# Kernel tuning notes

Hardware: AMD Instinct MI355X
Metric: run time of the kernel (lower is better)

The kernel has to match this reference:

```python
import jax, jax.numpy as jnp
import numpy as np

N_NODES = 100000
N_EDGES = 1600000
N_FEAT = 500
N_CLASSES = 40


def gcn_conv(x, W, b, src, dst, n):
    """PyG GCNConv: add self-loops, symmetric deg normalization, linear + bias."""
    h = x @ W                                   # [n, out]
    loop = jnp.arange(n, dtype=src.dtype)
    s = jnp.concatenate([src, loop])            # sources incl. self-loops
    d = jnp.concatenate([dst, loop])            # destinations incl. self-loops
    deg = jax.ops.segment_sum(jnp.ones_like(d, dtype=x.dtype), d, num_segments=n)
    dinv = jax.lax.rsqrt(deg)                   # deg >= 1 because of self-loops
    norm = dinv[s] * dinv[d]                    # [E+n]
    out = jax.ops.segment_sum(h[s] * norm[:, None], d, num_segments=n)
    return out + b


def glorot(key, fan_in, fan_out):
    lim = np.sqrt(6.0 / (fan_in + fan_out)).astype(np.float32)
    return jax.random.uniform(key, (fan_in, fan_out), jnp.float32, -lim, lim)


def setup_inputs() -> dict:
    key = jax.random.key(0)
    ks = jax.random.split(key, 6)
    x = jax.random.normal(ks[0], (N_NODES, N_FEAT), dtype=jnp.float32)
    edge_index = jax.random.randint(ks[1], (2, N_EDGES), 0, N_NODES, dtype=jnp.int64)
    return {
        "x": x,
        "edge_index": edge_index,
        "W1": glorot(ks[2], N_FEAT, 128), "b1": jnp.zeros((128,), jnp.float32),
        "W2": glorot(ks[3], 128, 64),     "b2": jnp.zeros((64,), jnp.float32),
        "W4": glorot(ks[4], 64, N_CLASSES), "b4": jnp.zeros((N_CLASSES,), jnp.float32),
    }


def reference(x, edge_index, W1, b1, W2, b2, W4, b4):
    src, dst = edge_index[0], edge_index[1]
    n = x.shape[0]
    h = jax.nn.relu(gcn_conv(x, W1, b1, src, dst, n))
    h = jax.nn.relu(gcn_conv(h, W2, b2, src, dst, n))
    h = gcn_conv(h, W4, b4, src, dst, n)
    return jax.nn.log_softmax(h, axis=1)
```

## Files before the change

### kernel.cpp

```cpp
#include <hip/hip_runtime.h>
#include <hip/hip_bf16.h>
#include <cmath>

#define NNODES 100000
#define NEDGES 1600000
#define SCAN_B 1024

typedef __attribute__((ext_vector_type(8))) short bf16x8;
typedef __attribute__((ext_vector_type(4))) float f32x4;

__device__ __forceinline__ unsigned short f2bf(float f) {
    unsigned u = __builtin_bit_cast(unsigned, f);
    unsigned r = (u + 0x7fffu + ((u >> 16) & 1u)) >> 16;
    return (unsigned short)r;
}
__device__ __forceinline__ float bflo(unsigned v) {
    return __builtin_bit_cast(float, v << 16);
}
__device__ __forceinline__ float bfhi(unsigned v) {
    return __builtin_bit_cast(float, v & 0xffff0000u);
}


__global__ void zero_deg(int* __restrict__ deg, int n) {
    int i = blockIdx.x * 256 + threadIdx.x;
    if (i < n) deg[i] = 0;
}

__global__ void count_deg(const int* __restrict__ dst, int* __restrict__ deg, int E) {
    int e = blockIdx.x * 256 + threadIdx.x;
    if (e < E) atomicAdd(&deg[dst[e]], 1);
}

__global__ void calc_dinv(const int* __restrict__ deg, float* __restrict__ dinv, int n) {
    int i = blockIdx.x * 256 + threadIdx.x;
    if (i < n) dinv[i] = rsqrtf(1.0f + (float)deg[i]);
}

__global__ __launch_bounds__(SCAN_B) void scan_block(const int* __restrict__ deg,
                                                     int* __restrict__ pos,
                                                     int* __restrict__ bsums, int n) {
    __shared__ int s[SCAN_B];
    int tid = threadIdx.x;
    int gid = blockIdx.x * SCAN_B + tid;
    int v = (gid < n) ? deg[gid] : 0;
    s[tid] = v;
    __syncthreads();
    for (int off = 1; off < SCAN_B; off <<= 1) {
        int t = (tid >= off) ? s[tid - off] : 0;
        __syncthreads();
        s[tid] += t;
        __syncthreads();
    }
    if (gid < n) pos[gid] = s[tid] - v;
    if (tid == SCAN_B - 1) bsums[blockIdx.x] = s[tid];
}

__global__ __launch_bounds__(128) void scan_sums(int* __restrict__ bsums, int nb) {
    __shared__ int s[128];
    int tid = threadIdx.x;
    int v = (tid < nb) ? bsums[tid] : 0;
    s[tid] = v;
    __syncthreads();
    for (int off = 1; off < 128; off <<= 1) {
        int t = (tid >= off) ? s[tid - off] : 0;
        __syncthreads();
        s[tid] += t;
        __syncthreads();
    }
    if (tid < nb) bsums[tid] = s[tid] - v;
}

__global__ __launch_bounds__(SCAN_B) void add_off(int* __restrict__ pos,
                                                  const int* __restrict__ bsums, int n) {
    int gid = blockIdx.x * SCAN_B + threadIdx.x;
    if (gid < n) pos[gid] += bsums[blockIdx.x];
}

__global__ void csr_fill(const int* __restrict__ src, const int* __restrict__ dst,
                         int* __restrict__ pos, int* __restrict__ csr_src, int E) {
    int e = blockIdx.x * 256 + threadIdx.x;
    if (e < E) {
        int slot = atomicAdd(&pos[dst[e]], 1);
        csr_src[slot] = src[e];
    }
}


__global__ __launch_bounds__(256) void conv_w1t(const float* __restrict__ W1,
                                                unsigned short* __restrict__ W1t) {
    int t = blockIdx.x * 256 + threadIdx.x;
    if (t >= 128 * 512) return;
    int n = t >> 9, k = t & 511;
    W1t[t] = (k < 500) ? f2bf(W1[k * 128 + n]) : (unsigned short)0;
}

__global__ __launch_bounds__(256) void conv_w2t(const float* __restrict__ W2,
                                                unsigned short* __restrict__ W2t) {
    int t = blockIdx.x * 256 + threadIdx.x;
    if (t >= 64 * 128) return;
    int n = t >> 7, k = t & 127;
    W2t[t] = f2bf(W2[k * 64 + n]);
}


__global__ __launch_bounds__(256) void gemm1_mfma(
    const float* __restrict__ x, const unsigned short* __restrict__ W1t,
    const float* __restrict__ dinv, unsigned short* __restrict__ C, int M)
{
    __shared__ short sA[4096];
    __shared__ short sB[4096];
    const int tid = threadIdx.x;
    const int w = tid >> 6;
    const int l = tid & 63;
    const int lm = l & 15;
    const int q = l >> 4;
    const int row0 = blockIdx.x * 128;

    f32x4 acc[2][8];
    #pragma unroll
    for (int i = 0; i < 2; i++)
        #pragma unroll
        for (int j = 0; j < 8; j++) acc[i][j] = (f32x4){0.f, 0.f, 0.f, 0.f};

    for (int k0 = 0; k0 < 512; k0 += 32) {
        __syncthreads();
        #pragma unroll
        for (int rep = 0; rep < 2; rep++) {
            int b = tid + rep * 256;
            int qq = b >> 7, m = b & 127;
            int r = row0 + m; if (r >= M) r = M - 1;
            int kb = k0 + qq * 8;
            bf16x8 o;
            if (kb + 8 <= 500) {
                float4 u = *(const float4*)(x + (size_t)r * 500 + kb);
                float4 v = *(const float4*)(x + (size_t)r * 500 + kb + 4);
                o[0] = f2bf(u.x); o[1] = f2bf(u.y); o[2] = f2bf(u.z); o[3] = f2bf(u.w);
                o[4] = f2bf(v.x); o[5] = f2bf(v.y); o[6] = f2bf(v.z); o[7] = f2bf(v.w);
            } else {
                #pragma unroll
                for (int j = 0; j < 8; j++) {
                    int k = kb + j;
                    o[j] = (k < 500) ? (short)f2bf(x[(size_t)r * 500 + k]) : (short)0;
                }
            }
            *(bf16x8*)&sA[b * 8] = o;
        }
        #pragma unroll
        for (int rep = 0; rep < 2; rep++) {
            int b = tid + rep * 256;
            int qq = b >> 7, n = b & 127;
            bf16x8 v = *(const bf16x8*)(W1t + (size_t)n * 512 + k0 + qq * 8);
            *(bf16x8*)&sB[b * 8] = v;
        }
        __syncthreads();
        bf16x8 af[2];
        #pragma unroll
        for (int i = 0; i < 2; i++)
            af[i] = *(const bf16x8*)&sA[(q * 128 + w * 32 + i * 16 + lm) * 8];
        bf16x8 bfr[8];
        #pragma unroll
        for (int j = 0; j < 8; j++)
            bfr[j] = *(const bf16x8*)&sB[(q * 128 + j * 16 + lm) * 8];
        #pragma unroll
        for (int i = 0; i < 2; i++)
            #pragma unroll
            for (int j = 0; j < 8; j++)
                acc[i][j] = __builtin_amdgcn_mfma_f32_16x16x32_bf16(af[i], bfr[j], acc[i][j], 0, 0, 0);
    }

    #pragma unroll
    for (int i = 0; i < 2; i++) {
        #pragma unroll
        for (int reg = 0; reg < 4; reg++) {
            int grow = row0 + w * 32 + i * 16 + q * 4 + reg;
            if (grow < M) {
                float d = dinv[grow];
                #pragma unroll
                for (int j = 0; j < 8; j++)
                    C[(size_t)grow * 128 + j * 16 + lm] = f2bf(d * acc[i][j][reg]);
            }
        }
    }
}


__global__ __launch_bounds__(256) void gemm2_mfma(
    const unsigned short* __restrict__ A, const unsigned short* __restrict__ Bt,
    const float* __restrict__ dinv, unsigned short* __restrict__ C, int M)
{
    __shared__ short sA[4096];
    __shared__ short sB[2048];
    const int tid = threadIdx.x;
    const int w = tid >> 6;
    const int l = tid & 63;
    const int lm = l & 15;
    const int q = l >> 4;
    const int row0 = blockIdx.x * 128;

    f32x4 acc[2][4];
    #pragma unroll
    for (int i = 0; i < 2; i++)
        #pragma unroll
        for (int j = 0; j < 4; j++) acc[i][j] = (f32x4){0.f, 0.f, 0.f, 0.f};

    for (int k0 = 0; k0 < 128; k0 += 32) {
        __syncthreads();
        #pragma unroll
        for (int rep = 0; rep < 2; rep++) {
            int b = tid + rep * 256;
            int qq = b >> 7, m = b & 127;
            int r = row0 + m; if (r >= M) r = M - 1;
            *(bf16x8*)&sA[b * 8] = *(const bf16x8*)(A + (size_t)r * 128 + k0 + qq * 8);
        }
        {
            int b = tid;
            int qq = b >> 6, n = b & 63;
            *(bf16x8*)&sB[b * 8] = *(const bf16x8*)(Bt + (size_t)n * 128 + k0 + qq * 8);
        }
        __syncthreads();
        bf16x8 af[2];
        #pragma unroll
        for (int i = 0; i < 2; i++)
            af[i] = *(const bf16x8*)&sA[(q * 128 + w * 32 + i * 16 + lm) * 8];
        bf16x8 bfr[4];
        #pragma unroll
        for (int j = 0; j < 4; j++)
            bfr[j] = *(const bf16x8*)&sB[(q * 64 + j * 16 + lm) * 8];
        #pragma unroll
        for (int i = 0; i < 2; i++)
            #pragma unroll
            for (int j = 0; j < 4; j++)
                acc[i][j] = __builtin_amdgcn_mfma_f32_16x16x32_bf16(af[i], bfr[j], acc[i][j], 0, 0, 0);
    }

    #pragma unroll
    for (int i = 0; i < 2; i++) {
        #pragma unroll
        for (int reg = 0; reg < 4; reg++) {
            int grow = row0 + w * 32 + i * 16 + q * 4 + reg;
            if (grow < M) {
                float d = dinv[grow];
                #pragma unroll
                for (int j = 0; j < 4; j++)
                    C[(size_t)grow * 64 + j * 16 + lm] = f2bf(d * acc[i][j][reg]);
            }
        }
    }
}


__global__ __launch_bounds__(256) void gemm_n40(
    const float* __restrict__ A, const float* __restrict__ W,
    const float* __restrict__ bias, const float* __restrict__ dinv,
    float* __restrict__ C, int M)
{
    __shared__ float sA[32][65];
    __shared__ float sW[64][40];
    const int row0 = blockIdx.x * 32;
    for (int idx = threadIdx.x; idx < 64 * 40; idx += 256)
        sW[idx / 40][idx % 40] = W[idx];
    for (int idx = threadIdx.x; idx < 32 * 64; idx += 256) {
        int r = idx >> 6, k = idx & 63;
        int row = row0 + r;
        float v = 0.0f;
        if (row < M) v = fmaxf(A[(long)row * 64 + k] + bias[k], 0.0f);
        sA[r][k] = v;
    }
    __syncthreads();
    float acc[5] = {0, 0, 0, 0, 0};
    int rr[5], cc[5];
    #pragma unroll
    for (int j = 0; j < 5; j++) {
        int o = threadIdx.x + 256 * j;
        rr[j] = o / 40; cc[j] = o % 40;
    }
    for (int k = 0; k < 64; k++) {
        #pragma unroll
        for (int j = 0; j < 5; j++) acc[j] += sA[rr[j]][k] * sW[k][cc[j]];
    }
    #pragma unroll
    for (int j = 0; j < 5; j++) {
        int row = row0 + rr[j];
        if (row < M) C[(long)row * 40 + cc[j]] = dinv[row] * acc[j];
    }
}


template<int F, bool OBF16>
__global__ __launch_bounds__(256) void gather_bf(
    const unsigned short* __restrict__ h, const float* __restrict__ dinv,
    const int* __restrict__ pos, const int* __restrict__ csr_src,
    void* __restrict__ outv, const float* __restrict__ bias, int n)
{
    constexpr int P = F / 2;
    unsigned t = blockIdx.x * 256u + threadIdx.x;
    unsigned node = t / P;
    unsigned p = t - node * P;
    if (node >= (unsigned)n) return;
    int e0 = node ? pos[node - 1] : 0;
    int e1 = pos[node];
    float di = dinv[node];
    unsigned sv = *(const unsigned*)(h + (size_t)node * F + 2 * p);
    float a0 = bflo(sv);
    float a1 = bfhi(sv);
    int j = e0;
    for (; j + 4 <= e1; j += 4) {
        int s0 = csr_src[j], s1 = csr_src[j + 1], s2 = csr_src[j + 2], s3 = csr_src[j + 3];
        unsigned v0 = *(const unsigned*)(h + (size_t)s0 * F + 2 * p);
        unsigned v1 = *(const unsigned*)(h + (size_t)s1 * F + 2 * p);
        unsigned v2 = *(const unsigned*)(h + (size_t)s2 * F + 2 * p);
        unsigned v3 = *(const unsigned*)(h + (size_t)s3 * F + 2 * p);
        a0 += bflo(v0) + bflo(v1) + bflo(v2) + bflo(v3);
        a1 += bfhi(v0) + bfhi(v1) + bfhi(v2) + bfhi(v3);
    }
    for (; j < e1; j++) {
        int s = csr_src[j];
        unsigned v = *(const unsigned*)(h + (size_t)s * F + 2 * p);
        a0 += bflo(v);
        a1 += bfhi(v);
    }
    a0 *= di; a1 *= di;
    if constexpr (OBF16) {
        a0 = fmaxf(a0 + bias[2 * p], 0.0f);
        a1 = fmaxf(a1 + bias[2 * p + 1], 0.0f);
        ((unsigned*)outv)[(size_t)node * P + p] =
            ((unsigned)f2bf(a1) << 16) | (unsigned)f2bf(a0);
    } else {
        float2 r; r.x = a0; r.y = a1;
        ((float2*)outv)[(size_t)node * P + p] = r;
    }
}


template<int F>
__global__ __launch_bounds__(256) void gather_agg(
    const float* __restrict__ h, const float* __restrict__ dinv,
    const int* __restrict__ pos, const int* __restrict__ csr_src,
    float* __restrict__ out, int n)
{
    unsigned t = blockIdx.x * 256u + threadIdx.x;
    unsigned node = t / F;
    unsigned c = t - node * F;
    if (node >= (unsigned)n) return;
    int e0 = node ? pos[node - 1] : 0;
    int e1 = pos[node];
    float di = dinv[node];
    float acc = h[(size_t)node * F + c];
    int j = e0;
    for (; j + 4 <= e1; j += 4) {
        int s0 = csr_src[j], s1 = csr_src[j + 1], s2 = csr_src[j + 2], s3 = csr_src[j + 3];
        float v0 = h[(size_t)s0 * F + c];
        float v1 = h[(size_t)s1 * F + c];
        float v2 = h[(size_t)s2 * F + c];
        float v3 = h[(size_t)s3 * F + c];
        acc += v0 + v1 + v2 + v3;
    }
    for (; j < e1; j++) {
        int s = csr_src[j];
        acc += h[(size_t)s * F + c];
    }
    out[(size_t)node * F + c] = di * acc;
}


__global__ __launch_bounds__(256) void logsoftmax40(const float* __restrict__ h,
                                                    const float* __restrict__ bias,
                                                    float* __restrict__ out, int n) {
    int wave = (blockIdx.x * 256 + threadIdx.x) >> 6;
    int lane = threadIdx.x & 63;
    if (wave >= n) return;
    float x = 0.0f, v = -INFINITY;
    if (lane < 40) { x = h[(long)wave * 40 + lane] + bias[lane]; v = x; }
    #pragma unroll
    for (int off = 32; off; off >>= 1) v = fmaxf(v, __shfl_xor(v, off, 64));
    float ex = (lane < 40) ? expf(x - v) : 0.0f;
    float s = ex;
    #pragma unroll
    for (int off = 32; off; off >>= 1) s += __shfl_xor(s, off, 64);
    if (lane < 40) out[(long)wave * 40 + lane] = x - v - logf(s);
}


extern "C" void kernel_launch(void* const* d_in, const int* in_sizes, int n_in,
                              void* d_out, int out_size, void* d_ws, size_t ws_size,
                              hipStream_t stream) {
    const float* x  = (const float*)d_in[0];
    const int*   ei = (const int*)d_in[1];
    const float* W1 = (const float*)d_in[2];
    const float* b1 = (const float*)d_in[3];
    const float* W2 = (const float*)d_in[4];
    const float* b2 = (const float*)d_in[5];
    const float* W4 = (const float*)d_in[6];
    const float* b4 = (const float*)d_in[7];
    float* out = (float*)d_out;
    float* ws  = (float*)d_ws;

    const int N = NNODES, E = NEDGES;
    const int* src = ei;
    const int* dst = ei + E;

    float*          dinv    = ws;
    int*            deg     = (int*)(ws + 100000);
    int*            pos     = (int*)(ws + 200000);
    int*            bsums   = (int*)(ws + 300000);
    int*            csr_src = (int*)(ws + 300200);
    unsigned short* W1t     = (unsigned short*)(ws + 1900200);
    unsigned short* W2t     = (unsigned short*)(ws + 1933000);
    unsigned short* h1      = (unsigned short*)(ws + 1937100);
    unsigned short* h2      = (unsigned short*)(ws + 1937100);
    unsigned short* a1      = (unsigned short*)(ws + 8337100);
    float*          h3      = ws + 8337100;
    float*          a2      = ws + 14737100;
    float*          a3      = out;

    const int nscan = (N + SCAN_B - 1) / SCAN_B;

    zero_deg<<<(N + 255) / 256, 256, 0, stream>>>(deg, N);
    count_deg<<<(E + 255) / 256, 256, 0, stream>>>(dst, deg, E);
    calc_dinv<<<(N + 255) / 256, 256, 0, stream>>>(deg, dinv, N);
    scan_block<<<nscan, SCAN_B, 0, stream>>>(deg, pos, bsums, N);
    scan_sums<<<1, 128, 0, stream>>>(bsums, nscan);
    add_off<<<nscan, SCAN_B, 0, stream>>>(pos, bsums, N);
    csr_fill<<<(E + 255) / 256, 256, 0, stream>>>(src, dst, pos, csr_src, E);

    conv_w1t<<<(128 * 512 + 255) / 256, 256, 0, stream>>>(W1, W1t);
    conv_w2t<<<(64 * 128 + 255) / 256, 256, 0, stream>>>(W2, W2t);

    gemm1_mfma<<<(N + 127) / 128, 256, 0, stream>>>(x, W1t, dinv, h1, N);
    {
        unsigned tot = (unsigned)N * 64u;
        gather_bf<128, true><<<(tot + 255) / 256, 256, 0, stream>>>(h1, dinv, pos, csr_src, a1, b1, N);
    }

    gemm2_mfma<<<(N + 127) / 128, 256, 0, stream>>>(a1, W2t, dinv, h2, N);
    {
        unsigned tot = (unsigned)N * 32u;
        gather_bf<64, false><<<(tot + 255) / 256, 256, 0, stream>>>(h2, dinv, pos, csr_src, a2, nullptr, N);
    }

    gemm_n40<<<(N + 31) / 32, 256, 0, stream>>>(a2, W4, b2, dinv, h3, N);
    {
        unsigned tot = (unsigned)N * 40u;
        gather_agg<40><<<(tot + 255) / 256, 256, 0, stream>>>(h3, dinv, pos, csr_src, a3, N);
    }

    logsoftmax40<<<(N * 64 + 255) / 256, 256, 0, stream>>>(a3, b4, out, N);
}
```

Measured before the change: 820.5 us.

## Partition degree counting and CSR fill by XCD-local destination ranges

Degree counting and CSR fill now use 1024 blocks grouped by blockIdx mod 8, on the assumption that consecutive blocks are spread round-robin across the 8 XCDs. Each group scans the whole edge list but only performs atomics for destinations in its own eighth of the node range. The aim is to keep each node's atomics inside one XCD's L2 and avoid cross-die coherence traffic. In exchange, every edge's dst is read eight times and src loads become divergent, and the benefit depends on the block-to-XCD mapping holding.

```diff
diff --git a/kernel.cpp b/kernel.cpp
--- a/kernel.cpp
+++ b/kernel.cpp
@@ -27,9 +27,16 @@
     if (i < n) deg[i] = 0;
 }
 
-__global__ void count_deg(const int* __restrict__ dst, int* __restrict__ deg, int E) {
-    int e = blockIdx.x * 256 + threadIdx.x;
-    if (e < E) atomicAdd(&deg[dst[e]], 1);
+__global__ __launch_bounds__(256) void count_deg_xcd(const int* __restrict__ dst,
+                                                     int* __restrict__ deg, int E) {
+    int g = blockIdx.x & 7;
+    int sub = blockIdx.x >> 3;
+    int nsub = gridDim.x >> 3;
+    int lo = g * (NNODES / 8), hi = lo + (NNODES / 8);
+    for (int e = sub * 256 + threadIdx.x; e < E; e += nsub * 256) {
+        int d = dst[e];
+        if (d >= lo && d < hi) atomicAdd(&deg[d], 1);
+    }
 }
 
 __global__ void calc_dinv(const int* __restrict__ deg, float* __restrict__ dinv, int n) {
@@ -77,12 +84,20 @@
     if (gid < n) pos[gid] += bsums[blockIdx.x];
 }
 
-__global__ void csr_fill(const int* __restrict__ src, const int* __restrict__ dst,
-                         int* __restrict__ pos, int* __restrict__ csr_src, int E) {
-    int e = blockIdx.x * 256 + threadIdx.x;
-    if (e < E) {
-        int slot = atomicAdd(&pos[dst[e]], 1);
-        csr_src[slot] = src[e];
+__global__ __launch_bounds__(256) void csr_fill_xcd(const int* __restrict__ src,
+                                                    const int* __restrict__ dst,
+                                                    int* __restrict__ pos,
+                                                    int* __restrict__ csr_src, int E) {
+    int g = blockIdx.x & 7;
+    int sub = blockIdx.x >> 3;
+    int nsub = gridDim.x >> 3;
+    int lo = g * (NNODES / 8), hi = lo + (NNODES / 8);
+    for (int e = sub * 256 + threadIdx.x; e < E; e += nsub * 256) {
+        int d = dst[e];
+        if (d >= lo && d < hi) {
+            int slot = atomicAdd(&pos[d], 1);
+            csr_src[slot] = src[e];
+        }
     }
 }
 
@@ -417,12 +432,12 @@
     const int nscan = (N + SCAN_B - 1) / SCAN_B;
 
     zero_deg<<<(N + 255) / 256, 256, 0, stream>>>(deg, N);
-    count_deg<<<(E + 255) / 256, 256, 0, stream>>>(dst, deg, E);
+    count_deg_xcd<<<1024, 256, 0, stream>>>(dst, deg, E);
     calc_dinv<<<(N + 255) / 256, 256, 0, stream>>>(deg, dinv, N);
     scan_block<<<nscan, SCAN_B, 0, stream>>>(deg, pos, bsums, N);
     scan_sums<<<1, 128, 0, stream>>>(bsums, nscan);
     add_off<<<nscan, SCAN_B, 0, stream>>>(pos, bsums, N);
-    csr_fill<<<(E + 255) / 256, 256, 0, stream>>>(src, dst, pos, csr_src, E);
+    csr_fill_xcd<<<1024, 256, 0, stream>>>(src, dst, pos, csr_src, E);
 
     conv_w1t<<<(128 * 512 + 255) / 256, 256, 0, stream>>>(W1, W1t);
     conv_w2t<<<(64 * 128 + 255) / 256, 256, 0, stream>>>(W2, W2t);
```

After: 772.3 us. -5.9%, faster.
